# Kernel optimization log

Hardware: AMD Instinct MI355X
Metric: run time of the kernel (lower is better)

## Reference

```python
import jax, jax.numpy as jnp
import numpy as np


def _bitlinear(x, W, b):
    # BitNet 1.58 absmean ternary quantization with STE.
    gamma = jnp.abs(W).mean() + 1e-8
    w_tern = jnp.clip(jnp.round(W / gamma), -1.0, 1.0)
    # STE: forward uses ternary weights, gradient flows to W.
    w_ste = w_tern + (W - jax.lax.stop_gradient(W))
    return x @ w_ste.T + b


def _gelu(x):
    return jax.nn.gelu(x, approximate=False)  # torch nn.GELU default is exact erf


def setup_inputs() -> dict:
    key = jax.random.key(0)
    ks = jax.random.split(key, 16)
    B, H = 8192, 2048
    dims = [2048, 1024, 512, 256]  # encoder: 2048->1024->512->256
    inp = {
        "z": jax.random.normal(ks[0], (B, H // 2), jnp.float32),
        "attention_out": jax.random.normal(ks[1], (B, H // 2), jnp.float32),
    }
    ki = 2
    for l in range(3):
        inp[f"We{l}"] = jax.random.normal(ks[ki], (dims[l + 1], dims[l]), jnp.float32) * 0.02
        inp[f"be{l}"] = jnp.zeros((dims[l + 1],), jnp.float32)
        ki += 1
    inp["Wb"] = jax.random.normal(ks[ki], (256, 256), jnp.float32) * 0.02
    inp["bb"] = jnp.zeros((256,), jnp.float32)
    ki += 1
    for l in range(3):  # decoder: 256->512->1024->2048
        inp[f"Wd{l}"] = jax.random.normal(ks[ki], (dims[2 - l], dims[3 - l]), jnp.float32) * 0.02
        inp[f"bd{l}"] = jnp.zeros((dims[2 - l],), jnp.float32)
        ki += 1
    return inp


def reference(z, attention_out, We0, be0, We1, be1, We2, be2, Wb, bb,
              Wd0, bd0, Wd1, bd1, Wd2, bd2):
    x = jnp.concatenate([z, attention_out], axis=-1)  # (B, 2048)
    skips = []
    for W, b in [(We0, be0), (We1, be1), (We2, be2)]:
        x = _gelu(_bitlinear(x, W, b))
        skips.append(x)
    x = _gelu(_bitlinear(x, Wb, bb))
    for i, (W, b) in enumerate([(Wd0, bd0), (Wd1, bd1), (Wd2, bd2)]):
        x = _bitlinear(x, W, b)
        skip = skips[-(i + 1)]
        if x.shape[-1] == skip.shape[-1]:  # static dim check; never true for this config
            x = x + skip
        x = _gelu(x)
    return x
```

## Files before the change

### kernel.cpp

```cpp
#include <hip/hip_runtime.h>
#include <hip/hip_bf16.h>
#include <cstdint>

typedef __attribute__((ext_vector_type(8))) __bf16 bf16x8;
typedef __attribute__((ext_vector_type(4))) float f32x4;

typedef __attribute__((address_space(1))) const void g_void;
typedef __attribute__((address_space(3))) void l_void;

__device__ __forceinline__ void gload_lds16(const void* g, void* l) {
  __builtin_amdgcn_global_load_lds((g_void*)(uintptr_t)g,
                                   (l_void*)(uint32_t)(uintptr_t)l, 16, 0, 0);
}

__device__ __forceinline__ ushort f2bf(float f) {
  union { float f; uint32_t u; } v; v.f = f;
  uint32_t r = v.u + 0x7fffu + ((v.u >> 16) & 1u);
  return (ushort)(r >> 16);
}

struct WDesc {
  const float* W[7];
  int nvec[7];
  int vcum[8];
};

__global__ void absmean_partial(WDesc wd, float* __restrict__ partials) {
  __shared__ float red[256];
  const int layer = blockIdx.y;
  const float4* W = (const float4*)wd.W[layer];
  const int nv = wd.nvec[layer];
  float s = 0.f;
  for (int i = blockIdx.x * 256 + threadIdx.x; i < nv; i += gridDim.x * 256) {
    float4 w = W[i];
    s += fabsf(w.x) + fabsf(w.y) + fabsf(w.z) + fabsf(w.w);
  }
  red[threadIdx.x] = s;
  __syncthreads();
  for (int o = 128; o > 0; o >>= 1) {
    if (threadIdx.x < o) red[threadIdx.x] += red[threadIdx.x + o];
    __syncthreads();
  }
  if (threadIdx.x == 0) partials[layer * 64 + blockIdx.x] = red[0];
}

__global__ void absmean_final(WDesc wd, const float* __restrict__ partials,
                              float* __restrict__ ig) {
  const int layer = blockIdx.x;
  float v = partials[layer * 64 + threadIdx.x];
  for (int o = 32; o > 0; o >>= 1) v += __shfl_down(v, o, 64);
  if (threadIdx.x == 0) {
    float mean = v / (float)(wd.nvec[layer] * 4);
    ig[layer] = 1.0f / (mean + 1e-8f);
  }
}

__global__ void prep_kernel(WDesc wd, const float* __restrict__ ig,
                            ushort* __restrict__ qw,
                            const float* __restrict__ z,
                            const float* __restrict__ att,
                            ushort* __restrict__ cat, int qblks) {
  if ((int)blockIdx.x < qblks) {
    const int v = blockIdx.x * 256 + threadIdx.x;
    if (v >= wd.vcum[7]) return;
    int layer = 0;
#pragma unroll
    for (int i = 1; i < 7; ++i) layer += (v >= wd.vcum[i]);
    const int lv = v - wd.vcum[layer];
    const float g = ig[layer];
    float4 w = ((const float4*)wd.W[layer])[lv];
    ushort4 o;
    o.x = f2bf(fmaxf(-1.f, fminf(1.f, rintf(w.x * g))));
    o.y = f2bf(fmaxf(-1.f, fminf(1.f, rintf(w.y * g))));
    o.z = f2bf(fmaxf(-1.f, fminf(1.f, rintf(w.z * g))));
    o.w = f2bf(fmaxf(-1.f, fminf(1.f, rintf(w.w * g))));
    ((ushort4*)qw)[v] = o;
  } else {
    const int tg = (blockIdx.x - qblks) * 256 + threadIdx.x;
    const int row = tg >> 8;
    const int k0 = (tg & 255) * 8;
    const float* src = (k0 < 1024) ? (z + (size_t)row * 1024 + k0)
                                   : (att + (size_t)row * 1024 + (k0 - 1024));
    float4 a = ((const float4*)src)[0];
    float4 b = ((const float4*)src)[1];
    ushort4 o0; o0.x = f2bf(a.x); o0.y = f2bf(a.y); o0.z = f2bf(a.z); o0.w = f2bf(a.w);
    ushort4 o1; o1.x = f2bf(b.x); o1.y = f2bf(b.y); o1.z = f2bf(b.z); o1.w = f2bf(b.w);
    ushort4* dst = (ushort4*)(cat + (size_t)tg * 8);
    dst[0] = o0; dst[1] = o1;
  }
}

__device__ __forceinline__ float gelu_fast(float x) {
  float x2 = x * x;
  float u = x * fmaf(x2, 0.0356774081f, 0.7978845608f);
  float e = exp2f(u * 2.8853900818f);
  float r = __builtin_amdgcn_rcpf(e + 1.0f);
  return x - x * r;
}

#define SB0() __builtin_amdgcn_sched_barrier(0)
#define BAR() __builtin_amdgcn_s_barrier()
#define LGKM0() asm volatile("s_waitcnt lgkmcnt(0)" ::: "memory")
#define VMW(NN) asm volatile("s_waitcnt vmcnt(%0)" ::"n"(NN) : "memory")

template <int BN, bool OUT_F32>
__global__ __launch_bounds__(512, 2)
void gemm_pipe3(const ushort* __restrict__ A, const ushort* __restrict__ Bw,
                const float* __restrict__ bias, void* __restrict__ Cv,
                int M, int N, int K) {
  constexpr int BM = 256;
  constexpr int WN = BN / 4;
  constexpr int FM = 8;
  constexpr int FN = WN / 16;
  constexpr int HM = 4;
  constexpr int HN = 1;
  constexpr int SA = 4;
  constexpr int SB = BN / 64;
  constexpr int L = SA + SB;
  constexpr int TILE_USH = (BM + BN) * 64;

  __shared__ ushort lds[3 * TILE_USH];

  const int t = threadIdx.x;
  const int lane = t & 63, wid = t >> 6;
  const int wr = wid >> 2, wc = wid & 3;
  const int l15 = lane & 15, lhi = lane >> 4;

  const int gx = gridDim.x;
  const int nwg = gx * gridDim.y;
  int lin = blockIdx.y * gx + blockIdx.x;
  lin = (lin & 7) * (nwg >> 3) + (lin >> 3);
  const int bm0 = (lin / gx) * BM, bn0 = (lin % gx) * BN;

  const int NT = K >> 6;

  const int srow = t >> 3;
  const int scol = ((t & 7) ^ ((t >> 3) & 7)) * 8;

  auto stage = [&](int tile, int buf) {
    ushort* tb = &lds[buf * TILE_USH];
    const int kt = tile * 64;
#pragma unroll
    for (int c = 0; c < SA; ++c) {
      const int lr = c * 64 + srow;
      gload_lds16(A + (size_t)(bm0 + lr) * K + kt + scol,
                  &tb[lr * 64 + (t & 7) * 8]);
    }
#pragma unroll
    for (int c = 0; c < SB; ++c) {
      const int lr = c * 64 + srow;
      gload_lds16(Bw + (size_t)(bn0 + lr) * K + kt + scol,
                  &tb[BM * 64 + lr * 64 + (t & 7) * 8]);
    }
  };

  bf16x8 a[HM][2], b[HN][2];
  f32x4 acc[FM][FN] = {};

  auto loadA = [&](const ushort* tb, int mh) {
#pragma unroll
    for (int mi = 0; mi < HM; ++mi) {
      const int row = wr * 128 + (mh * HM + mi) * 16 + l15;
#pragma unroll
      for (int kh = 0; kh < 2; ++kh)
        a[mi][kh] =
            *(const bf16x8*)&tb[row * 64 + ((kh * 4 + lhi) ^ (l15 & 7)) * 8];
    }
  };
  auto loadB = [&](const ushort* tb, int nh) {
#pragma unroll
    for (int ni = 0; ni < HN; ++ni) {
      const int row = wc * WN + (nh * HN + ni) * 16 + l15;
#pragma unroll
      for (int kh = 0; kh < 2; ++kh)
        b[ni][kh] = *(const bf16x8*)&tb[BM * 64 + row * 64 +
                                        ((kh * 4 + lhi) ^ (l15 & 7)) * 8];
    }
  };

#define MFMA_(MH, NH)                                                        \
  {                                                                          \
    __builtin_amdgcn_s_setprio(1);                                           \
    _Pragma("unroll") for (int kh = 0; kh < 2; ++kh)                         \
    _Pragma("unroll") for (int mi = 0; mi < HM; ++mi)                        \
    _Pragma("unroll") for (int ni = 0; ni < HN; ++ni)                        \
      acc[(MH) * HM + mi][(NH) * HN + ni] =                                  \
          __builtin_amdgcn_mfma_f32_16x16x32_bf16(                           \
              a[mi][kh], b[ni][kh], acc[(MH) * HM + mi][(NH) * HN + ni],     \
              0, 0, 0);                                                      \
    __builtin_amdgcn_s_setprio(0);                                           \
  }

  stage(0, 0);
  stage(1, 1);
  VMW(L);
  BAR();
  SB0();

  int buf = 0, sbuf = 2;
  for (int tt = 0; tt < NT; ++tt) {
    const bool more = (tt + 2 < NT);
    if (more) stage(tt + 2, sbuf);
    const ushort* tb = &lds[buf * TILE_USH];
    if constexpr (FN == 2) {
      loadA(tb, 0); loadB(tb, 0);
      MFMA_(0, 0);
      loadB(tb, 1);
      MFMA_(0, 1);
      loadA(tb, 1);
      MFMA_(1, 1);
      loadB(tb, 0);
      MFMA_(1, 0);
    } else {
      loadA(tb, 0); loadB(tb, 0);
      MFMA_(0, 0);
      loadA(tb, 1);
      MFMA_(1, 0);
    }
    SB0();
    if (more) { VMW(L); } else { VMW(0); }
    BAR();
    SB0();
    buf = (buf == 2) ? 0 : buf + 1;
    sbuf = (sbuf == 2) ? 0 : sbuf + 1;
  }
#undef MFMA_

#pragma unroll
  for (int n = 0; n < FN; ++n) {
    const int col = bn0 + wc * WN + n * 16 + l15;
    const float bv = bias[col];
#pragma unroll
    for (int m = 0; m < FM; ++m) {
      const int row0 = bm0 + wr * 128 + m * 16 + lhi * 4;
#pragma unroll
      for (int j = 0; j < 4; ++j) {
        float v = acc[m][n][j] + bv;
        float gv = gelu_fast(v);
        if (OUT_F32)
          ((float*)Cv)[(size_t)(row0 + j) * N + col] = gv;
        else
          ((ushort*)Cv)[(size_t)(row0 + j) * N + col] = f2bf(gv);
      }
    }
  }
}

template <int BN, bool OUT_F32>
__global__ __launch_bounds__(512, 2)
void gemm_half(const ushort* __restrict__ A, const ushort* __restrict__ Bw,
               const float* __restrict__ bias, void* __restrict__ Cv,
               int M, int N, int K) {
  constexpr int BM = 256;
  constexpr int WN = BN / 4;
  constexpr int FM = 8;
  constexpr int FN = WN / 16;
  constexpr int HM = 4;
  constexpr int HN = FN / 2;
  constexpr int SA = 4;
  constexpr int SB = BN / 64;
  constexpr int L = SA + SB;
  constexpr int TILE_USH = (BM + BN) * 64;

  __shared__ ushort lds[2 * TILE_USH];

  const int t = threadIdx.x;
  const int lane = t & 63, wid = t >> 6;
  const int wr = wid >> 2, wc = wid & 3;
  const int l15 = lane & 15, lhi = lane >> 4;

  const int gx = gridDim.x;
  const int nwg = gx * gridDim.y;
  int lin = blockIdx.y * gx + blockIdx.x;
  lin = (lin & 7) * (nwg >> 3) + (lin >> 3);
  const int bm0 = (lin / gx) * BM, bn0 = (lin % gx) * BN;

  const int NT = K >> 6;

  const int srow = t >> 3;
  const int scol = ((t & 7) ^ ((t >> 3) & 7)) * 8;

  auto stage = [&](int tile, int buf) {
    ushort* tb = &lds[buf * TILE_USH];
    const int kt = tile * 64;
#pragma unroll
    for (int c = 0; c < SA; ++c) {
      const int lr = c * 64 + srow;
      gload_lds16(A + (size_t)(bm0 + lr) * K + kt + scol,
                  &tb[lr * 64 + (t & 7) * 8]);
    }
#pragma unroll
    for (int c = 0; c < SB; ++c) {
      const int lr = c * 64 + srow;
      gload_lds16(Bw + (size_t)(bn0 + lr) * K + kt + scol,
                  &tb[BM * 64 + lr * 64 + (t & 7) * 8]);
    }
  };

  bf16x8 a[HM][2], b[HN][2];
  f32x4 acc[FM][FN] = {};

  auto loadA = [&](const ushort* tb, int mh) {
#pragma unroll
    for (int mi = 0; mi < HM; ++mi) {
      const int row = wr * 128 + (mh * HM + mi) * 16 + l15;
#pragma unroll
      for (int kh = 0; kh < 2; ++kh)
        a[mi][kh] =
            *(const bf16x8*)&tb[row * 64 + ((kh * 4 + lhi) ^ (l15 & 7)) * 8];
    }
  };
  auto loadB = [&](const ushort* tb, int nh) {
#pragma unroll
    for (int ni = 0; ni < HN; ++ni) {
      const int row = wc * WN + (nh * HN + ni) * 16 + l15;
#pragma unroll
      for (int kh = 0; kh < 2; ++kh)
        b[ni][kh] = *(const bf16x8*)&tb[BM * 64 + row * 64 +
                                        ((kh * 4 + lhi) ^ (l15 & 7)) * 8];
    }
  };

#define MFMA_(MH, NH)                                                        \
  {                                                                          \
    __builtin_amdgcn_s_setprio(1);                                           \
    _Pragma("unroll") for (int kh = 0; kh < 2; ++kh)                         \
    _Pragma("unroll") for (int mi = 0; mi < HM; ++mi)                        \
    _Pragma("unroll") for (int ni = 0; ni < HN; ++ni)                        \
      acc[(MH) * HM + mi][(NH) * HN + ni] =                                  \
          __builtin_amdgcn_mfma_f32_16x16x32_bf16(                           \
              a[mi][kh], b[ni][kh], acc[(MH) * HM + mi][(NH) * HN + ni],     \
              0, 0, 0);                                                      \
    __builtin_amdgcn_s_setprio(0);                                           \
  }

#define TILE_(P, TT)                                                         \
  {                                                                          \
    const bool more = (TT) + 2 < NT;                                         \
    const ushort* tb = &lds[(P) * TILE_USH];                                 \
    loadA(tb, 0); loadB(tb, 0);                                              \
    MFMA_(0, 0);                                                             \
    loadB(tb, 1);                                                            \
    MFMA_(0, 1);                                                             \
    loadA(tb, 1);                                                            \
    MFMA_(1, 1);                                                             \
    loadB(tb, 0);                                                            \
    LGKM0();                                                                 \
    BAR();                                                                   \
    SB0();                                                                   \
    if (more) stage((TT) + 2, P);                                            \
    MFMA_(1, 0);                                                             \
    SB0();                                                                   \
    if (more) { VMW(L); } else { VMW(0); }                                   \
    BAR();                                                                   \
    SB0();                                                                   \
  }

  stage(0, 0);
  stage(1, 1);
  VMW(L);
  BAR();
  SB0();

  for (int it = 0; it < (NT >> 1); ++it) {
    TILE_(0, 2 * it);
    TILE_(1, 2 * it + 1);
  }
#undef TILE_
#undef MFMA_

#pragma unroll
  for (int n = 0; n < FN; ++n) {
    const int col = bn0 + wc * WN + n * 16 + l15;
    const float bv = bias[col];
#pragma unroll
    for (int m = 0; m < FM; ++m) {
      const int row0 = bm0 + wr * 128 + m * 16 + lhi * 4;
#pragma unroll
      for (int j = 0; j < 4; ++j) {
        float v = acc[m][n][j] + bv;
        float gv = gelu_fast(v);
        if (OUT_F32)
          ((float*)Cv)[(size_t)(row0 + j) * N + col] = gv;
        else
          ((ushort*)Cv)[(size_t)(row0 + j) * N + col] = f2bf(gv);
      }
    }
  }
}

template <int BM, int BN, bool OUT_F32>
__global__ __launch_bounds__(256, 4)
void gemm_bt_bias_gelu(const ushort* __restrict__ A, const ushort* __restrict__ Bw,
                       const float* __restrict__ bias, void* __restrict__ Cv,
                       int M, int N, int K) {
  constexpr int WTM = BM / 32;
  constexpr int WTN = BN / 32;
  __shared__ ushort As[BM * 64];
  __shared__ ushort Bs[BN * 64];
  const int t = threadIdx.x;
  const int lane = t & 63, wid = t >> 6;
  const int wr = wid >> 1, wc = wid & 1;
  const int l15 = lane & 15, lhi = lane >> 4;

  const int gx = gridDim.x;
  const int nwg = gx * gridDim.y;
  int lin = blockIdx.y * gx + blockIdx.x;
  if ((nwg & 7) == 0) lin = (lin & 7) * (nwg >> 3) + (lin >> 3);
  const int bm0 = (lin / gx) * BM, bn0 = (lin % gx) * BN;

  const ushort* Abase = A + (size_t)bm0 * K;
  const ushort* Bbase = Bw + (size_t)bn0 * K;

  f32x4 acc[WTM][WTN] = {};

  for (int kt = 0; kt < K; kt += 64) {
#pragma unroll
    for (int i = 0; i < BM / 32; ++i) {
      int c = i * 256 + t;
      int r = c >> 3, c8 = c & 7;
      gload_lds16(Abase + (size_t)r * K + kt + c8 * 8, &As[c * 8]);
    }
#pragma unroll
    for (int i = 0; i < BN / 32; ++i) {
      int c = i * 256 + t;
      int r = c >> 3, c8 = c & 7;
      gload_lds16(Bbase + (size_t)r * K + kt + c8 * 8, &Bs[c * 8]);
    }
    asm volatile("s_waitcnt vmcnt(0)" ::: "memory");
    __syncthreads();
#pragma unroll
    for (int kk = 0; kk < 64; kk += 32) {
      bf16x8 af[WTM], bfr[WTN];
#pragma unroll
      for (int m = 0; m < WTM; ++m)
        af[m] = *(const bf16x8*)&As[(wr * (BM / 2) + m * 16 + l15) * 64 + kk + lhi * 8];
#pragma unroll
      for (int n = 0; n < WTN; ++n)
        bfr[n] = *(const bf16x8*)&Bs[(wc * (BN / 2) + n * 16 + l15) * 64 + kk + lhi * 8];
#pragma unroll
      for (int m = 0; m < WTM; ++m)
#pragma unroll
        for (int n = 0; n < WTN; ++n)
          acc[m][n] = __builtin_amdgcn_mfma_f32_16x16x32_bf16(af[m], bfr[n], acc[m][n], 0, 0, 0);
    }
    __syncthreads();
  }

#pragma unroll
  for (int n = 0; n < WTN; ++n) {
    const int col = bn0 + wc * (BN / 2) + n * 16 + l15;
    const float bv = bias[col];
#pragma unroll
    for (int m = 0; m < WTM; ++m) {
      const int row0 = bm0 + wr * (BM / 2) + m * 16 + lhi * 4;
#pragma unroll
      for (int j = 0; j < 4; ++j) {
        float v = acc[m][n][j] + bv;
        float gv = gelu_fast(v);
        if (OUT_F32)
          ((float*)Cv)[(size_t)(row0 + j) * N + col] = gv;
        else
          ((ushort*)Cv)[(size_t)(row0 + j) * N + col] = f2bf(gv);
      }
    }
  }
}

extern "C" void kernel_launch(void* const* d_in, const int* in_sizes, int n_in,
                              void* d_out, int out_size, void* d_ws, size_t ws_size,
                              hipStream_t stream) {
  const float* z   = (const float*)d_in[0];
  const float* att = (const float*)d_in[1];
  const float* Wptr[7] = {(const float*)d_in[2],  (const float*)d_in[4],
                          (const float*)d_in[6],  (const float*)d_in[8],
                          (const float*)d_in[10], (const float*)d_in[12],
                          (const float*)d_in[14]};
  const float* bptr[7] = {(const float*)d_in[3],  (const float*)d_in[5],
                          (const float*)d_in[7],  (const float*)d_in[9],
                          (const float*)d_in[11], (const float*)d_in[13],
                          (const float*)d_in[15]};
  const int Ns[7] = {1024, 512, 256, 256, 512, 1024, 2048};
  const int Ks[7] = {2048, 1024, 512, 256, 256, 512, 1024};
  const int M = 8192;

  char* ws = (char*)d_ws;
  ushort* bufA = (ushort*)ws;
  ushort* bufB = (ushort*)(ws + 33554432);
  ushort* qw   = (ushort*)(ws + 33554432 + 16777216);
  float* partials = (float*)(ws + 33554432 + 16777216 + 11141120);
  float* ig = partials + 7 * 64;

  WDesc wd;
  int cum = 0;
  size_t qoff[7]; size_t qc = 0;
  for (int l = 0; l < 7; ++l) {
    wd.W[l] = Wptr[l];
    int nv = Ns[l] * Ks[l] / 4;
    wd.nvec[l] = nv;
    wd.vcum[l] = cum;
    cum += nv;
    qoff[l] = qc;
    qc += (size_t)Ns[l] * Ks[l];
  }
  wd.vcum[7] = cum;

  const int qblks = (cum + 255) / 256;
  absmean_partial<<<dim3(64, 7), 256, 0, stream>>>(wd, partials);
  absmean_final<<<7, 64, 0, stream>>>(wd, partials, ig);
  prep_kernel<<<qblks + 8192, 256, 0, stream>>>(wd, ig, qw, z, att, bufA, qblks);

  ushort* inb = bufA; ushort* outb = bufB;
  gemm_pipe3<128, false><<<dim3(Ns[0] / 128, M / 256), dim3(512), 0, stream>>>(
      inb, qw + qoff[0], bptr[0], outb, M, Ns[0], Ks[0]);
  { ushort* tmp = inb; inb = outb; outb = tmp; }
  gemm_pipe3<64, false><<<dim3(Ns[1] / 64, M / 256), dim3(512), 0, stream>>>(
      inb, qw + qoff[1], bptr[1], outb, M, Ns[1], Ks[1]);
  { ushort* tmp = inb; inb = outb; outb = tmp; }
  gemm_bt_bias_gelu<64, 64, false><<<dim3(Ns[2] / 64, M / 64), 256, 0, stream>>>(
      inb, qw + qoff[2], bptr[2], outb, M, Ns[2], Ks[2]);
  { ushort* tmp = inb; inb = outb; outb = tmp; }
  gemm_bt_bias_gelu<64, 64, false><<<dim3(Ns[3] / 64, M / 64), 256, 0, stream>>>(
      inb, qw + qoff[3], bptr[3], outb, M, Ns[3], Ks[3]);
  { ushort* tmp = inb; inb = outb; outb = tmp; }
  gemm_pipe3<64, false><<<dim3(Ns[4] / 64, M / 256), dim3(512), 0, stream>>>(
      inb, qw + qoff[4], bptr[4], outb, M, Ns[4], Ks[4]);
  { ushort* tmp = inb; inb = outb; outb = tmp; }
  gemm_pipe3<128, false><<<dim3(Ns[5] / 128, M / 256), dim3(512), 0, stream>>>(
      inb, qw + qoff[5], bptr[5], outb, M, Ns[5], Ks[5]);
  { ushort* tmp = inb; inb = outb; outb = tmp; }
  gemm_bt_bias_gelu<128, 128, true><<<dim3(Ns[6] / 128, M / 128), 256, 0, stream>>>(
      inb, qw + qoff[6], bptr[6], d_out, M, Ns[6], Ks[6]);
}
```

Measured before the change: 186.6 us.

## Use 256x256 eight-phase pipelined GEMM for final decoder layer

```diff
diff --git a/kernel.cpp b/kernel.cpp
--- a/kernel.cpp
+++ b/kernel.cpp
@@ -246,20 +246,18 @@
   }
 }
 
-template <int BN, bool OUT_F32>
-__global__ __launch_bounds__(512, 2)
-void gemm_half(const ushort* __restrict__ A, const ushort* __restrict__ Bw,
-               const float* __restrict__ bias, void* __restrict__ Cv,
-               int M, int N, int K) {
+template <bool OUT_F32>
+__global__ __launch_bounds__(512, 1)
+void gemm_8ph(const ushort* __restrict__ A, const ushort* __restrict__ Bw,
+              const float* __restrict__ bias, void* __restrict__ Cv,
+              int M, int N, int K) {
   constexpr int BM = 256;
-  constexpr int WN = BN / 4;
+  constexpr int BN = 256;
+  constexpr int WN = 64;
   constexpr int FM = 8;
-  constexpr int FN = WN / 16;
+  constexpr int FN = 4;
   constexpr int HM = 4;
-  constexpr int HN = FN / 2;
-  constexpr int SA = 4;
-  constexpr int SB = BN / 64;
-  constexpr int L = SA + SB;
+  constexpr int HN = 2;
   constexpr int TILE_USH = (BM + BN) * 64;
 
   __shared__ ushort lds[2 * TILE_USH];
@@ -280,18 +278,18 @@
   const int srow = t >> 3;
   const int scol = ((t & 7) ^ ((t >> 3) & 7)) * 8;
 
-  auto stage = [&](int tile, int buf) {
-    ushort* tb = &lds[buf * TILE_USH];
-    const int kt = tile * 64;
-#pragma unroll
-    for (int c = 0; c < SA; ++c) {
-      const int lr = c * 64 + srow;
+  auto stageA2 = [&](ushort* tb, int kt, int h) {
+#pragma unroll
+    for (int c = 0; c < 2; ++c) {
+      const int lr = h * 128 + c * 64 + srow;
       gload_lds16(A + (size_t)(bm0 + lr) * K + kt + scol,
                   &tb[lr * 64 + (t & 7) * 8]);
     }
-#pragma unroll
-    for (int c = 0; c < SB; ++c) {
-      const int lr = c * 64 + srow;
+  };
+  auto stageB2 = [&](ushort* tb, int kt, int h) {
+#pragma unroll
+    for (int c = 0; c < 2; ++c) {
+      const int lr = h * 128 + c * 64 + srow;
       gload_lds16(Bw + (size_t)(bn0 + lr) * K + kt + scol,
                   &tb[BM * 64 + lr * 64 + (t & 7) * 8]);
     }
@@ -334,39 +332,63 @@
     __builtin_amdgcn_s_setprio(0);                                           \
   }
 
-#define TILE_(P, TT)                                                         \
-  {                                                                          \
-    const bool more = (TT) + 2 < NT;                                         \
-    const ushort* tb = &lds[(P) * TILE_USH];                                 \
-    loadA(tb, 0); loadB(tb, 0);                                              \
-    MFMA_(0, 0);                                                             \
-    loadB(tb, 1);                                                            \
-    MFMA_(0, 1);                                                             \
-    loadA(tb, 1);                                                            \
-    MFMA_(1, 1);                                                             \
-    loadB(tb, 0);                                                            \
-    LGKM0();                                                                 \
-    BAR();                                                                   \
-    SB0();                                                                   \
-    if (more) stage((TT) + 2, P);                                            \
-    MFMA_(1, 0);                                                             \
-    SB0();                                                                   \
-    if (more) { VMW(L); } else { VMW(0); }                                   \
-    BAR();                                                                   \
-    SB0();                                                                   \
-  }
-
-  stage(0, 0);
-  stage(1, 1);
-  VMW(L);
+  stageB2(&lds[0], 0, 0);
+  stageB2(&lds[0], 0, 1);
+  stageA2(&lds[0], 0, 0);
+  stageA2(&lds[0], 0, 1);
+  VMW(2);
   BAR();
   SB0();
 
-  for (int it = 0; it < (NT >> 1); ++it) {
-    TILE_(0, 2 * it);
-    TILE_(1, 2 * it + 1);
-  }
-#undef TILE_
+  for (int J = 0; J < NT; ++J) {
+    const ushort* tb = &lds[(J & 1) * TILE_USH];
+    ushort* sb = &lds[((J & 1) ^ 1) * TILE_USH];
+    const int kt2 = (J + 1) << 6;
+    const bool more = (J + 1) < NT;
+
+    loadA(tb, 0);
+    loadB(tb, 0);
+    if (more) stageB2(sb, kt2, 0);
+    BAR();
+    LGKM0();
+    SB0();
+    MFMA_(0, 0);
+    SB0();
+    BAR();
+    SB0();
+
+    loadB(tb, 1);
+    if (more) stageB2(sb, kt2, 1);
+    BAR();
+    LGKM0();
+    SB0();
+    MFMA_(0, 1);
+    SB0();
+    if (more) { VMW(4); } else { VMW(0); }
+    BAR();
+    SB0();
+
+    loadA(tb, 1);
+    if (more) stageA2(sb, kt2, 0);
+    BAR();
+    LGKM0();
+    SB0();
+    MFMA_(1, 1);
+    SB0();
+    BAR();
+    SB0();
+
+    loadB(tb, 0);
+    if (more) stageA2(sb, kt2, 1);
+    BAR();
+    LGKM0();
+    SB0();
+    MFMA_(1, 0);
+    SB0();
+    if (more) { VMW(2); } else { VMW(0); }
+    BAR();
+    SB0();
+  }
 #undef MFMA_
 
 #pragma unroll
@@ -529,6 +551,6 @@
   gemm_pipe3<128, false><<<dim3(Ns[5] / 128, M / 256), dim3(512), 0, stream>>>(
       inb, qw + qoff[5], bptr[5], outb, M, Ns[5], Ks[5]);
   { ushort* tmp = inb; inb = outb; outb = tmp; }
-  gemm_bt_bias_gelu<128, 128, true><<<dim3(Ns[6] / 128, M / 128), 256, 0, stream>>>(
+  gemm_8ph<true><<<dim3(Ns[6] / 256, M / 256), dim3(512), 0, stream>>>(
       inb, qw + qoff[6], bptr[6], d_out, M, Ns[6], Ks[6]);
 }
```

Result: no change. 186.2 us (-0.2%).
